# Kernel optimization log

Measured on AMD Instinct MI355X. Metric: run time of the kernel, lower is better.

The kernel has to match this reference:

```python
import jax, jax.numpy as jnp
import numpy as np

V, D_IN = 32000, 300      # vocab, embedding dim (GRU input_size=300)
N, T = 4096, 64           # total nodes across batched graphs, tokens per node
B, NPG = 64, 64           # graphs, nodes per graph
E = 65536                 # total edges (avg degree 16)
RH, GH = 256, 256         # rnn_hidden_dim, gnn_hidden_dim


def gru_cell(x_proj, h, W_hh, b_hh):
    # x_proj = x @ W_ih.T + b_ih, shape [N, 3H]; PyTorch GRU gate order (r, z, n)
    gh = h @ W_hh.T + b_hh
    xr, xz, xn = jnp.split(x_proj, 3, axis=-1)
    hr, hz, hn = jnp.split(gh, 3, axis=-1)
    r = jax.nn.sigmoid(xr + hr)
    z = jax.nn.sigmoid(xz + hz)
    n = jnp.tanh(xn + r * hn)
    return (1.0 - z) * n + z * h


def setup_inputs() -> dict:
    key = jax.random.key(0)
    ks = jax.random.split(key, 16)
    tokens = jax.random.randint(ks[0], (N, T), 0, V)
    # edges live within a single graph (dgl.batch keeps graphs disjoint)
    edge_graph = jnp.arange(E) // (E // B)
    edge_src = edge_graph * NPG + jax.random.randint(ks[1], (E,), 0, NPG)
    edge_dst = edge_graph * NPG + jax.random.randint(ks[2], (E,), 0, NPG)
    graph_id = jnp.arange(N) // NPG
    local = jnp.arange(N) % NPG
    # node types: 0=history, 1=last_sentence (one per graph), 2=response (one per graph)
    node_type = jnp.where(local == NPG - 2, 1, jnp.where(local == NPG - 1, 2, 0))
    s = 0.02
    p = lambda k, shape: jax.random.normal(k, shape, dtype=jnp.float32) * s
    return dict(
        tokens=tokens, edge_src=edge_src, edge_dst=edge_dst,
        graph_id=graph_id, node_type=node_type,
        emb_table=p(ks[3], (V, D_IN)),
        W_ih_f=p(ks[4], (3 * RH, D_IN)), W_hh_f=p(ks[5], (3 * RH, RH)),
        b_ih_f=jnp.zeros((3 * RH,), jnp.float32), b_hh_f=jnp.zeros((3 * RH,), jnp.float32),
        W_ih_b=p(ks[6], (3 * RH, D_IN)), W_hh_b=p(ks[7], (3 * RH, RH)),
        b_ih_b=jnp.zeros((3 * RH,), jnp.float32), b_hh_b=jnp.zeros((3 * RH,), jnp.float32),
        W_g1=p(ks[8], (2 * RH, GH)), b_g1=jnp.zeros((GH,), jnp.float32),
        W_g2=p(ks[9], (GH, GH)), b_g2=jnp.zeros((GH,), jnp.float32),
        W_g3=p(ks[10], (GH, GH)), b_g3=jnp.zeros((GH,), jnp.float32),
        W_g4=p(ks[11], (GH, GH)), b_g4=jnp.zeros((GH,), jnp.float32),
    )


def reference(tokens, edge_src, edge_dst, graph_id, node_type, emb_table,
              W_ih_f, W_hh_f, b_ih_f, b_hh_f,
              W_ih_b, W_hh_b, b_ih_b, b_hh_b,
              W_g1, b_g1, W_g2, b_g2, W_g3, b_g3, W_g4, b_g4):
    x = emb_table[tokens]  # [N, T, 300]
    # Module keeps only output[:, -1, :]:
    #   forward half  = final forward hidden state (full scan over T)
    #   backward half = backward state after processing only timestep T-1
    #                   (i.e. one GRU cell step from zero state) -- exact math.
    xp_f = jnp.einsum('ntd,gd->ntg', x, W_ih_f) + b_ih_f  # [N, T, 3H]
    h0 = jnp.zeros((N, RH), x.dtype)

    def step(h, xp_t):
        return gru_cell(xp_t, h, W_hh_f, b_hh_f), None

    h_fwd, _ = jax.lax.scan(step, h0, jnp.swapaxes(xp_f, 0, 1))
    xp_b = x[:, -1] @ W_ih_b.T + b_ih_b
    h_bwd = gru_cell(xp_b, h0, W_hh_b, b_hh_b)
    h = jnp.concatenate([h_fwd, h_bwd], axis=-1)  # [N, 2H]

    # 4 GCN layers: sum-aggregate neighbor features (copy_src -> sum), then linear + ReLU
    for W, b in ((W_g1, b_g1), (W_g2, b_g2), (W_g3, b_g3), (W_g4, b_g4)):
        agg = jax.ops.segment_sum(h[edge_src], edge_dst, num_segments=N)
        h = jax.nn.relu(agg @ W + b)

    # per-graph readout by node type
    hist_m = (node_type == 0).astype(h.dtype)[:, None]
    last_m = (node_type == 1).astype(h.dtype)[:, None]
    resp_m = (node_type == 2).astype(h.dtype)[:, None]
    hist_sum = jax.ops.segment_sum(h * hist_m, graph_id, num_segments=B)
    hist_cnt = jax.ops.segment_sum(hist_m, graph_id, num_segments=B)
    batched_hist = hist_sum / hist_cnt
    batched_last = jax.ops.segment_sum(h * last_m, graph_id, num_segments=B)
    batched_resp = jax.ops.segment_sum(h * resp_m, graph_id, num_segments=B)
    return (batched_hist, batched_last, batched_resp)
```

## Files before the change

kernel.cpp:

```cpp
#include <hip/hip_runtime.h>
#include <cstddef>

#define NN_ 4096
#define TT_ 64
#define DIN 300
#define DINP 320
#define RH_ 256
#define G3_ 768
#define BB_ 64
#define EE_ 65536

typedef short bf16x8 __attribute__((ext_vector_type(8)));
typedef float f32x4 __attribute__((ext_vector_type(4)));
typedef unsigned short u16;

__device__ __forceinline__ u16 f2bf(float f) {
    unsigned u = __builtin_bit_cast(unsigned, f);
    u += 0x7fff + ((u >> 16) & 1);
    return (u16)(u >> 16);
}
__device__ __forceinline__ float bf2f(u16 v) {
    return __builtin_bit_cast(float, (unsigned)v << 16);
}

__device__ __forceinline__ void gload16(const void* g, void* l) {
    __builtin_amdgcn_global_load_lds(
        (const __attribute__((address_space(1))) unsigned*)g,
        (__attribute__((address_space(3))) unsigned*)l, 16, 0, 0);
}

#define MFMA16 __builtin_amdgcn_mfma_f32_16x16x32_bf16

__global__ void k_zero(float* __restrict__ p, long n) {
    for (long i = (long)blockIdx.x * blockDim.x + threadIdx.x; i < n;
         i += (long)gridDim.x * blockDim.x)
        p[i] = 0.f;
}

__global__ void k_cvt(const float* __restrict__ src, u16* __restrict__ dst,
                      int R, int C, int Cp) {
    long total = (long)R * Cp;
    for (long i = (long)blockIdx.x * blockDim.x + threadIdx.x; i < total;
         i += (long)gridDim.x * blockDim.x) {
        int r = (int)(i / Cp);
        int c = (int)(i - (long)r * Cp);
        dst[i] = (c < C) ? f2bf(src[(size_t)r * C + c]) : (u16)0;
    }
}

__global__ void k_cvtT(const float* __restrict__ W, u16* __restrict__ Wt, int K) {
    int total = 256 * K;
    for (int i = blockIdx.x * blockDim.x + threadIdx.x; i < total;
         i += gridDim.x * blockDim.x) {
        int c = i / K, k = i - c * K;
        Wt[i] = f2bf(W[(size_t)k * 256 + c]);
    }
}

__global__ void k_buildA(const int* __restrict__ src, const int* __restrict__ dst,
                         float* __restrict__ A) {
    int e = blockIdx.x * blockDim.x + threadIdx.x;
    if (e < EE_) {
        int g = src[e] >> 6, i = dst[e] & 63, j = src[e] & 63;
        atomicAdd(&A[(((g << 6) + i) << 6) + j], 1.f);
    }
}

__global__ __launch_bounds__(256) void k_trans(const float* __restrict__ h, int C,
                                               u16* __restrict__ hT) {
    __shared__ u16 Ls[64][72];
    int r0 = blockIdx.x * 64, c0 = blockIdx.y * 64;
    int tid = threadIdx.x;
    int r = tid >> 2, cq = tid & 3;
#pragma unroll
    for (int i = 0; i < 4; i++) {
        float4 v = *(const float4*)(h + (size_t)(r0 + r) * C + c0 + cq * 16 + i * 4);
        Ls[r][cq * 16 + i * 4 + 0] = f2bf(v.x);
        Ls[r][cq * 16 + i * 4 + 1] = f2bf(v.y);
        Ls[r][cq * 16 + i * 4 + 2] = f2bf(v.z);
        Ls[r][cq * 16 + i * 4 + 3] = f2bf(v.w);
    }
    __syncthreads();
    int c = tid >> 2, rq = tid & 3;
    u16 tmp[16];
#pragma unroll
    for (int i = 0; i < 16; i++) tmp[i] = Ls[rq * 16 + i][c];
    u16* o = hT + (size_t)(c0 + c) * NN_ + r0 + rq * 16;
    *(uint4*)o = ((const uint4*)tmp)[0];
    *(uint4*)(o + 8) = ((const uint4*)tmp)[1];
}

__global__ __launch_bounds__(256) void k_xproj(
    const u16* __restrict__ embbf, const u16* __restrict__ Wx,
    const float* __restrict__ bih, const float* __restrict__ bhh,
    u16* __restrict__ XP)
{
    __shared__ __align__(16) u16 As[2][64 * 32];
    __shared__ __align__(16) u16 Bs[2][64 * 32];
    const int tid = threadIdx.x;
    const int v0 = blockIdx.x * 64, c0 = blockIdx.y * 64;
    const int sr = tid >> 2, sq = tid & 3;
    const u16* pa = embbf + (size_t)(v0 + sr) * DINP + sq * 8;
    const u16* pb = Wx + (size_t)(c0 + sr) * DINP + sq * 8;

    const int lane = tid & 63, wave = tid >> 6;
    const int wr = wave >> 1, wc = wave & 1;
    const int l15 = lane & 15, l4 = lane >> 4;
    const int aoff = (wr * 32 + l15) * 32 + l4 * 8;
    const int boff = (wc * 32 + l15) * 32 + l4 * 8;
    f32x4 acc[2][2] = {};

    gload16(pa, &As[0][tid * 8]);
    gload16(pb, &Bs[0][tid * 8]);
    __syncthreads();
    constexpr int NSK = DINP / 32;
#pragma unroll
    for (int s = 0; s < NSK; s++) {
        if (s + 1 < NSK) {
            gload16(pa + (s + 1) * 32, &As[(s + 1) & 1][tid * 8]);
            gload16(pb + (s + 1) * 32, &Bs[(s + 1) & 1][tid * 8]);
        }
        const int b = s & 1;
        bf16x8 a0 = *(const bf16x8*)&As[b][aoff];
        bf16x8 a1 = *(const bf16x8*)&As[b][aoff + 512];
        bf16x8 b0 = *(const bf16x8*)&Bs[b][boff];
        bf16x8 b1 = *(const bf16x8*)&Bs[b][boff + 512];
        acc[0][0] = MFMA16(a0, b0, acc[0][0], 0, 0, 0);
        acc[0][1] = MFMA16(a0, b1, acc[0][1], 0, 0, 0);
        acc[1][0] = MFMA16(a1, b0, acc[1][0], 0, 0, 0);
        acc[1][1] = MFMA16(a1, b1, acc[1][1], 0, 0, 0);
        __syncthreads();
    }
#pragma unroll
    for (int fj = 0; fj < 2; fj++) {
        const int c = c0 + wc * 32 + fj * 16 + l15;
        const float bb = bih[c] + (c < 512 ? bhh[c] : 0.f);
#pragma unroll
        for (int fi = 0; fi < 2; fi++)
#pragma unroll
            for (int rg = 0; rg < 4; rg++) {
                const int v = v0 + wr * 32 + fi * 16 + l4 * 4 + rg;
                XP[(size_t)v * G3_ + c] = f2bf(acc[fi][fj][rg] + bb);
            }
    }
}

__global__ __launch_bounds__(512, 2) void k_scan(
    const int* __restrict__ tokens,
    const u16* __restrict__ XPROJ,
    const u16* __restrict__ Wh,
    const float* __restrict__ bhh,
    float* __restrict__ HA)
{
    __shared__ __align__(16) u16 XPs[16 * G3_];
    __shared__ __align__(16) u16 hS[16 * RH_];
    __shared__ int toks[16 * TT_];

    const int tid = threadIdx.x;
    const int n0 = blockIdx.x * 16;
    const int lane = tid & 63, wave = tid >> 6;
    const int l15 = lane & 15, l4 = lane >> 4;
    const int c0w = wave * 32;

    toks[tid] = tokens[n0 * TT_ + tid];
    toks[512 + tid] = tokens[n0 * TT_ + 512 + tid];
    ((unsigned long long*)hS)[tid] = 0ull;
    ((unsigned long long*)hS)[512 + tid] = 0ull;

    bf16x8 Bv[3][2][8];
#pragma unroll
    for (int g = 0; g < 3; ++g)
#pragma unroll
        for (int f = 0; f < 2; ++f)
#pragma unroll
            for (int ks = 0; ks < 8; ++ks)
                Bv[g][f][ks] = *(const bf16x8*)(
                    Wh + (size_t)(g * 256 + c0w + f * 16 + l15) * RH_ + ks * 32 + l4 * 8);

    const float bhn0 = bhh[512 + c0w + l15];
    const float bhn1 = bhh[512 + c0w + 16 + l15];

    int srow[3], soff[3];
#pragma unroll
    for (int i = 0; i < 3; ++i) {
        int c = tid + i * 512;
        srow[i] = c / 96;
        soff[i] = (c - srow[i] * 96) * 8;
    }
    u16* sdst[3];
#pragma unroll
    for (int i = 0; i < 3; ++i) sdst[i] = XPs + (tid + i * 512) * 8;

    auto STAGE_XP = [&](int t) {
#pragma unroll
        for (int i = 0; i < 3; ++i) {
            int tok = toks[srow[i] * TT_ + t];
            gload16(XPROJ + (size_t)tok * G3_ + soff[i], sdst[i]);
        }
    };

    f32x4 hprev0 = {0.f, 0.f, 0.f, 0.f}, hprev1 = {0.f, 0.f, 0.f, 0.f};

    __syncthreads();

    STAGE_XP(0);
    __syncthreads();

    for (int t = 0; t < TT_; ++t) {
        f32x4 acc[3][2] = {};
#pragma unroll
        for (int ks = 0; ks < 8; ++ks) {
            const int aa = (l15 * 512 + ks * 64 + l4 * 16) ^ ((l15 & 7) << 4);
            bf16x8 a = *(const bf16x8*)((const char*)hS + aa);
#pragma unroll
            for (int g = 0; g < 3; ++g) {
                acc[g][0] = MFMA16(a, Bv[g][0][ks], acc[g][0], 0, 0, 0);
                acc[g][1] = MFMA16(a, Bv[g][1][ks], acc[g][1], 0, 0, 0);
            }
        }
        __syncthreads();

#pragma unroll
        for (int f = 0; f < 2; ++f) {
            const int cc = c0w + f * 16 + l15;
            const float bhn = f == 0 ? bhn0 : bhn1;
#pragma unroll
            for (int rg = 0; rg < 4; ++rg) {
                const int r = l4 * 4 + rg;
                const int xb = r * G3_ + cc;
                float xr = bf2f(XPs[xb]);
                float xz = bf2f(XPs[xb + 256]);
                float xn = bf2f(XPs[xb + 512]);
                float gr = f == 0 ? acc[0][0][rg] : acc[0][1][rg];
                float gz = f == 0 ? acc[1][0][rg] : acc[1][1][rg];
                float gn = f == 0 ? acc[2][0][rg] : acc[2][1][rg];
                float hp = f == 0 ? hprev0[rg] : hprev1[rg];
                float rr = 1.f / (1.f + __expf(-(xr + gr)));
                float zz = 1.f / (1.f + __expf(-(xz + gz)));
                float pre = xn + rr * (gn + bhn);
                float nv = 2.f / (1.f + __expf(-2.f * pre)) - 1.f;
                float hnew = (1.f - zz) * nv + zz * hp;
                if (f == 0) hprev0[rg] = hnew; else hprev1[rg] = hnew;
                if (t < TT_ - 1) {
                    const int ba = (r * 512 + cc * 2) ^ ((r & 7) << 4);
                    *(u16*)((char*)hS + ba) = f2bf(hnew);
                } else {
                    HA[(size_t)(n0 + r) * 512 + cc] = hnew;
                }
            }
        }
        __syncthreads();
        if (t < TT_ - 1) STAGE_XP(t + 1);
    }
}

template<bool XONLY>
__global__ __launch_bounds__(256) void k_step(
    const int* __restrict__ tokens, int t,
    const u16* __restrict__ embbf, const u16* __restrict__ Wx,
    const u16* __restrict__ Wh,
    const float* __restrict__ bih, const float* __restrict__ bhh,
    const u16* __restrict__ hbf_in, const float* __restrict__ hf_in,
    float* __restrict__ outf, int ostride, u16* __restrict__ outbf)
{
    constexpr int NSX = DINP / 32;
    constexpr int NS  = XONLY ? NSX : NSX + RH_ / 32;

    __shared__ __align__(16) u16 As[2][32 * 32];
    __shared__ __align__(16) u16 Bs[2][3 * 64 * 32];

    const int tid = threadIdx.x;
    const int n0 = blockIdx.x * 32;
    const int c0 = blockIdx.y * 64;

    const int sr = tid >> 2;
    const int sq = tid & 3;
    const int tok = (tid < 128) ? tokens[(n0 + sr) * TT_ + t] : 0;
    const u16* ax  = embbf + (size_t)tok * DINP + sq * 8;
    const u16* ah  = XONLY ? ax : hbf_in + (size_t)(n0 + sr) * RH_ + sq * 8;
    const u16* bx0 = Wx + (size_t)(0 * 256 + c0 + sr) * DINP + sq * 8;
    const u16* bx1 = Wx + (size_t)(1 * 256 + c0 + sr) * DINP + sq * 8;
    const u16* bx2 = Wx + (size_t)(2 * 256 + c0 + sr) * DINP + sq * 8;
    const u16* bh0 = XONLY ? ax : Wh + (size_t)(0 * 256 + c0 + sr) * RH_ + sq * 8;
    const u16* bh1 = XONLY ? ax : Wh + (size_t)(1 * 256 + c0 + sr) * RH_ + sq * 8;
    const u16* bh2 = XONLY ? ax : Wh + (size_t)(2 * 256 + c0 + sr) * RH_ + sq * 8;

    auto STAGE = [&](int b, int s) {
        u16* db = &Bs[b][tid * 8];
        if (s < NSX) {
            int kk = s * 32;
            if (tid < 128) gload16(ax + kk, &As[b][tid * 8]);
            gload16(bx0 + kk, db);
            gload16(bx1 + kk, db + 2048);
            gload16(bx2 + kk, db + 4096);
        } else {
            int kk = (s - NSX) * 32;
            if (tid < 128) gload16(ah + kk, &As[b][tid * 8]);
            gload16(bh0 + kk, db);
            gload16(bh1 + kk, db + 2048);
            gload16(bh2 + kk, db + 4096);
        }
    };

    const int lane = tid & 63;
    const int wave = tid >> 6;
    const int wr = wave >> 1, wc = wave & 1;
    const int l15 = lane & 15, l4 = lane >> 4;

    f32x4 aR[2] = {}, aZ[2] = {}, aXN[2] = {}, aHN[2] = {};

    const int aoff = (wr * 16 + l15) * 32 + l4 * 8;
    const int boff = (wc * 32 + l15) * 32 + l4 * 8;

    auto COMPUTE = [&](int b, bool xp) {
        bf16x8 a0 = *(const bf16x8*)&As[b][aoff];
        const u16* B = &Bs[b][0];
        bf16x8 r0 = *(const bf16x8*)&B[boff];
        bf16x8 r1 = *(const bf16x8*)&B[boff + 512];
        bf16x8 z0 = *(const bf16x8*)&B[2048 + boff];
        bf16x8 z1 = *(const bf16x8*)&B[2048 + boff + 512];
        bf16x8 n0f = *(const bf16x8*)&B[4096 + boff];
        bf16x8 n1f = *(const bf16x8*)&B[4096 + boff + 512];
        aR[0] = MFMA16(a0, r0, aR[0], 0, 0, 0);
        aR[1] = MFMA16(a0, r1, aR[1], 0, 0, 0);
        aZ[0] = MFMA16(a0, z0, aZ[0], 0, 0, 0);
        aZ[1] = MFMA16(a0, z1, aZ[1], 0, 0, 0);
        if (xp) {
            aXN[0] = MFMA16(a0, n0f, aXN[0], 0, 0, 0);
            aXN[1] = MFMA16(a0, n1f, aXN[1], 0, 0, 0);
        } else {
            aHN[0] = MFMA16(a0, n0f, aHN[0], 0, 0, 0);
            aHN[1] = MFMA16(a0, n1f, aHN[1], 0, 0, 0);
        }
    };

    STAGE(0, 0);
    __syncthreads();
#pragma unroll
    for (int s = 0; s < NS; ++s) {
        if (s + 1 < NS) STAGE((s + 1) & 1, s + 1);
        COMPUTE(s & 1, s < NSX);
        __syncthreads();
    }

#pragma unroll
    for (int fj = 0; fj < 2; ++fj) {
        const int c = c0 + wc * 32 + fj * 16 + l15;
        const float bR  = bih[c] + bhh[c];
        const float bZ  = bih[256 + c] + bhh[256 + c];
        const float bXN = bih[512 + c];
        const float bHN = bhh[512 + c];
#pragma unroll
        for (int rg = 0; rg < 4; ++rg) {
            const int n = n0 + wr * 16 + l4 * 4 + rg;
            float r  = 1.f / (1.f + __expf(-(aR[fj][rg] + bR)));
            float z  = 1.f / (1.f + __expf(-(aZ[fj][rg] + bZ)));
            float pre = aXN[fj][rg] + bXN + r * (aHN[fj][rg] + bHN);
            float nv = 2.f / (1.f + __expf(-2.f * pre)) - 1.f;
            float hp = XONLY ? 0.f : hf_in[(size_t)n * RH_ + c];
            float h  = (1.f - z) * nv + z * hp;
            outf[(size_t)n * ostride + c] = h;
            if (!XONLY) outbf[(size_t)n * RH_ + c] = f2bf(h);
        }
    }
}

__global__ __launch_bounds__(256) void k_agg(
    const u16* __restrict__ Abf, const u16* __restrict__ hT,
    u16* __restrict__ aggbf, int C)
{
    const int g = blockIdx.x, ct = blockIdx.y;
    const int lane = threadIdx.x & 63, wave = threadIdx.x >> 6;
    const int wi = wave >> 1, wcC = wave & 1;
    const int l15 = lane & 15, l4 = lane >> 4;
    f32x4 acc[2][2] = {};
#pragma unroll
    for (int kc = 0; kc < 2; kc++) {
        bf16x8 af[2], bf_[2];
#pragma unroll
        for (int fi = 0; fi < 2; fi++)
            af[fi] = *(const bf16x8*)(Abf + ((size_t)g * 64 + wi * 32 + fi * 16 + l15) * 64
                                      + kc * 32 + l4 * 8);
#pragma unroll
        for (int fj = 0; fj < 2; fj++)
            bf_[fj] = *(const bf16x8*)(hT + (size_t)(ct * 64 + wcC * 32 + fj * 16 + l15) * NN_
                                       + g * 64 + kc * 32 + l4 * 8);
#pragma unroll
        for (int fi = 0; fi < 2; fi++)
#pragma unroll
            for (int fj = 0; fj < 2; fj++)
                acc[fi][fj] = MFMA16(af[fi], bf_[fj], acc[fi][fj], 0, 0, 0);
    }
#pragma unroll
    for (int fi = 0; fi < 2; fi++)
#pragma unroll
        for (int fj = 0; fj < 2; fj++)
#pragma unroll
            for (int rg = 0; rg < 4; rg++) {
                int n = g * 64 + wi * 32 + fi * 16 + l4 * 4 + rg;
                int c = ct * 64 + wcC * 32 + fj * 16 + l15;
                aggbf[(size_t)n * C + c] = f2bf(acc[fi][fj][rg]);
            }
}

template<int K>
__global__ __launch_bounds__(256) void k_gcnM(
    const u16* __restrict__ Ag, const u16* __restrict__ Wt,
    const float* __restrict__ bias, float* __restrict__ outF)
{
    __shared__ __align__(16) u16 As[2][64 * 32];
    __shared__ __align__(16) u16 Bs[2][64 * 32];
    const int tid = threadIdx.x;
    const int n0 = blockIdx.x * 64, c0 = blockIdx.y * 64;
    const int sr = tid >> 2, sq = tid & 3;
    const u16* pa = Ag + (size_t)(n0 + sr) * K + sq * 8;
    const u16* pb = Wt + (size_t)(c0 + sr) * K + sq * 8;

    const int lane = tid & 63, wave = tid >> 6;
    const int wr = wave >> 1, wc = wave & 1;
    const int l15 = lane & 15, l4 = lane >> 4;
    const int aoff = (wr * 32 + l15) * 32 + l4 * 8;
    const int boff = (wc * 32 + l15) * 32 + l4 * 8;
    f32x4 acc[2][2] = {};

    gload16(pa, &As[0][tid * 8]);
    gload16(pb, &Bs[0][tid * 8]);
    __syncthreads();
    constexpr int NSK = K / 32;
#pragma unroll
    for (int s = 0; s < NSK; s++) {
        if (s + 1 < NSK) {
            gload16(pa + (s + 1) * 32, &As[(s + 1) & 1][tid * 8]);
            gload16(pb + (s + 1) * 32, &Bs[(s + 1) & 1][tid * 8]);
        }
        const int b = s & 1;
        bf16x8 a0 = *(const bf16x8*)&As[b][aoff];
        bf16x8 a1 = *(const bf16x8*)&As[b][aoff + 512];
        bf16x8 b0 = *(const bf16x8*)&Bs[b][boff];
        bf16x8 b1 = *(const bf16x8*)&Bs[b][boff + 512];
        acc[0][0] = MFMA16(a0, b0, acc[0][0], 0, 0, 0);
        acc[0][1] = MFMA16(a0, b1, acc[0][1], 0, 0, 0);
        acc[1][0] = MFMA16(a1, b0, acc[1][0], 0, 0, 0);
        acc[1][1] = MFMA16(a1, b1, acc[1][1], 0, 0, 0);
        __syncthreads();
    }
#pragma unroll
    for (int fj = 0; fj < 2; fj++) {
        const int c = c0 + wc * 32 + fj * 16 + l15;
        const float bb = bias[c];
#pragma unroll
        for (int fi = 0; fi < 2; fi++)
#pragma unroll
            for (int rg = 0; rg < 4; rg++) {
                const int n = n0 + wr * 32 + fi * 16 + l4 * 4 + rg;
                outF[(size_t)n * 256 + c] = fmaxf(acc[fi][fj][rg] + bb, 0.f);
            }
    }
}

__global__ void k_readout(const float* __restrict__ h, const int* __restrict__ gid,
                          const int* __restrict__ ntype, float* __restrict__ out,
                          float* __restrict__ cnt)
{
    for (int idx = blockIdx.x * blockDim.x + threadIdx.x; idx < NN_ * 256;
         idx += gridDim.x * blockDim.x) {
        int n = idx >> 8, c = idx & 255;
        float v = h[idx];
        int g = gid[n], t = ntype[n];
        if (t == 0) {
            atomicAdd(&out[g * 256 + c], v);
            if (c == 0) atomicAdd(&cnt[g], 1.f);
        } else if (t == 1) {
            atomicAdd(&out[16384 + g * 256 + c], v);
        } else {
            atomicAdd(&out[32768 + g * 256 + c], v);
        }
    }
}

__global__ void k_finalize(float* __restrict__ out, const float* __restrict__ cnt)
{
    int idx = blockIdx.x * blockDim.x + threadIdx.x;
    out[idx] /= cnt[idx >> 8];
}

extern "C" void kernel_launch(void* const* d_in, const int* in_sizes, int n_in,
                              void* d_out, int out_size, void* d_ws, size_t ws_size,
                              hipStream_t stream)
{
    const int*   tokens = (const int*)d_in[0];
    const int*   esrc   = (const int*)d_in[1];
    const int*   edst   = (const int*)d_in[2];
    const int*   gid    = (const int*)d_in[3];
    const int*   ntype  = (const int*)d_in[4];
    const float* emb    = (const float*)d_in[5];
    const float* W_ih_f = (const float*)d_in[6];
    const float* W_hh_f = (const float*)d_in[7];
    const float* b_ih_f = (const float*)d_in[8];
    const float* b_hh_f = (const float*)d_in[9];
    const float* W_ih_b = (const float*)d_in[10];
    const float* b_ih_b = (const float*)d_in[12];
    const float* b_hh_b = (const float*)d_in[13];
    const float* Wg[4]  = {(const float*)d_in[14], (const float*)d_in[16],
                           (const float*)d_in[18], (const float*)d_in[20]};
    const float* bg[4]  = {(const float*)d_in[15], (const float*)d_in[17],
                           (const float*)d_in[19], (const float*)d_in[21]};
    float* out = (float*)d_out;

    float* hF    = (float*)d_ws;
    u16*   embbf = (u16*)(hF + (size_t)NN_ * RH_);
    u16*   wxf   = embbf + 32000L * DINP;
    u16*   whf   = wxf + (size_t)G3_ * DINP;
    u16*   wxb   = whf + (size_t)G3_ * RH_;
    u16*   wtg   = wxb + (size_t)G3_ * DINP;
    u16*   Abf   = wtg + 256L * 512;
    u16*   hT    = Abf + 64L * 64 * 64;
    u16*   aggb  = hT + 512L * NN_;
    u16*   XPROJ = aggb + (size_t)NN_ * 512;
    float* Af    = (float*)(XPROJ + 32000L * G3_);
    float* HA    = Af + 64L * 64 * 64;
    float* CNT   = HA + (size_t)NN_ * 512;

    k_cvt<<<2048, 256, 0, stream>>>(emb, embbf, 32000, DIN, DINP);
    k_cvt<<<256, 256, 0, stream>>>(W_ih_f, wxf, G3_, DIN, DINP);
    k_cvt<<<256, 256, 0, stream>>>(W_hh_f, whf, G3_, RH_, RH_);
    k_cvt<<<256, 256, 0, stream>>>(W_ih_b, wxb, G3_, DIN, DINP);
    k_zero<<<256, 256, 0, stream>>>(Af, 64L * 64 * 64);
    k_buildA<<<256, 256, 0, stream>>>(esrc, edst, Af);
    k_cvt<<<256, 256, 0, stream>>>(Af, Abf, 64 * 64, 64, 64);

    k_xproj<<<dim3(500, 12), 256, 0, stream>>>(embbf, wxf, b_ih_f, b_hh_f, XPROJ);
    k_scan<<<256, 512, 0, stream>>>(tokens, XPROJ, whf, b_hh_f, HA);

    k_step<true><<<dim3(128, 4), 256, 0, stream>>>(
        tokens, TT_ - 1, embbf, wxb, nullptr, b_ih_b, b_hh_b,
        nullptr, nullptr, HA + 256, 512, nullptr);

    k_trans<<<dim3(64, 8), 256, 0, stream>>>(HA, 512, hT);
    for (int l = 0; l < 4; l++) {
        int K = (l == 0) ? 512 : 256;
        k_cvtT<<<128, 256, 0, stream>>>(Wg[l], wtg, K);
        k_agg<<<dim3(64, K / 64), 256, 0, stream>>>(Abf, hT, aggb, K);
        if (K == 512)
            k_gcnM<512><<<dim3(64, 4), 256, 0, stream>>>(aggb, wtg, bg[l], hF);
        else
            k_gcnM<256><<<dim3(64, 4), 256, 0, stream>>>(aggb, wtg, bg[l], hF);
        if (l < 3) k_trans<<<dim3(64, 4), 256, 0, stream>>>(hF, 256, hT);
    }

    k_zero<<<256, 256, 0, stream>>>(out, 49152);
    k_zero<<<1, 64, 0, stream>>>(CNT, 64);
    k_readout<<<2048, 256, 0, stream>>>(hF, gid, ntype, out, CNT);
    k_finalize<<<64, 256, 0, stream>>>(out, CNT);
}
```

Before: 400.0 us.

## Interleave XPROJ gates per column and load directly into registers in GRU scan

Reorders the precomputed input projection so the r/z/n values of each hidden column sit together (padded to 4 halves). The scan kernel then fetches them straight into registers with one 8-byte load per element and prefetches the next step before the barrier, which removes the LDS staging buffer and the global-to-LDS copy. The LDS swizzle for the hidden state is also changed and workspace buffers are aliased. The price is a larger XPROJ buffer (4 slots per column instead of 3) and uncoalesced scattered register loads on the serial critical path.

```diff
diff --git a/kernel.cpp b/kernel.cpp
--- a/kernel.cpp
+++ b/kernel.cpp
@@ -13,6 +13,7 @@
 typedef short bf16x8 __attribute__((ext_vector_type(8)));
 typedef float f32x4 __attribute__((ext_vector_type(4)));
 typedef unsigned short u16;
+typedef unsigned short u16x4 __attribute__((ext_vector_type(4)));
 
 __device__ __forceinline__ u16 f2bf(float f) {
     unsigned u = __builtin_bit_cast(unsigned, f);
@@ -93,7 +94,7 @@
 __global__ __launch_bounds__(256) void k_xproj(
     const u16* __restrict__ embbf, const u16* __restrict__ Wx,
     const float* __restrict__ bih, const float* __restrict__ bhh,
-    u16* __restrict__ XP)
+    u16* __restrict__ XP2)
 {
     __shared__ __align__(16) u16 As[2][64 * 32];
     __shared__ __align__(16) u16 Bs[2][64 * 32];
@@ -133,28 +134,29 @@
     }
 #pragma unroll
     for (int fj = 0; fj < 2; fj++) {
-        const int c = c0 + wc * 32 + fj * 16 + l15;
-        const float bb = bih[c] + (c < 512 ? bhh[c] : 0.f);
+        const int cf = c0 + wc * 32 + fj * 16 + l15;
+        const int g = cf >> 8, c = cf & 255;
+        const float bb = bih[cf] + (cf < 512 ? bhh[cf] : 0.f);
 #pragma unroll
         for (int fi = 0; fi < 2; fi++)
 #pragma unroll
             for (int rg = 0; rg < 4; rg++) {
                 const int v = v0 + wr * 32 + fi * 16 + l4 * 4 + rg;
-                XP[(size_t)v * G3_ + c] = f2bf(acc[fi][fj][rg] + bb);
+                XP2[((size_t)v * 256 + c) * 4 + g] = f2bf(acc[fi][fj][rg] + bb);
             }
     }
 }
 
-__global__ __launch_bounds__(512, 2) void k_scan(
+__global__ __launch_bounds__(512) __attribute__((amdgpu_waves_per_eu(2, 2)))
+void k_scan(
     const int* __restrict__ tokens,
-    const u16* __restrict__ XPROJ,
+    const u16* __restrict__ XP2,
     const u16* __restrict__ Wh,
     const float* __restrict__ bhh,
     float* __restrict__ HA)
 {
-    __shared__ __align__(16) u16 XPs[16 * G3_];
     __shared__ __align__(16) u16 hS[16 * RH_];
-    __shared__ int toks[16 * TT_];
+    __shared__ int toks[16 * 68];
 
     const int tid = threadIdx.x;
     const int n0 = blockIdx.x * 16;
@@ -162,8 +164,10 @@
     const int l15 = lane & 15, l4 = lane >> 4;
     const int c0w = wave * 32;
 
-    toks[tid] = tokens[n0 * TT_ + tid];
-    toks[512 + tid] = tokens[n0 * TT_ + 512 + tid];
+    for (int idx = tid; idx < 16 * TT_; idx += 512) {
+        int row = idx >> 6, tt = idx & 63;
+        toks[row * 68 + tt] = tokens[(n0 + row) * TT_ + tt];
+    }
     ((unsigned long long*)hS)[tid] = 0ull;
     ((unsigned long long*)hS)[512 + tid] = 0ull;
 
@@ -180,37 +184,25 @@
     const float bhn0 = bhh[512 + c0w + l15];
     const float bhn1 = bhh[512 + c0w + 16 + l15];
 
-    int srow[3], soff[3];
-#pragma unroll
-    for (int i = 0; i < 3; ++i) {
-        int c = tid + i * 512;
-        srow[i] = c / 96;
-        soff[i] = (c - srow[i] * 96) * 8;
-    }
-    u16* sdst[3];
-#pragma unroll
-    for (int i = 0; i < 3; ++i) sdst[i] = XPs + (tid + i * 512) * 8;
-
-    auto STAGE_XP = [&](int t) {
-#pragma unroll
-        for (int i = 0; i < 3; ++i) {
-            int tok = toks[srow[i] * TT_ + t];
-            gload16(XPROJ + (size_t)tok * G3_ + soff[i], sdst[i]);
-        }
-    };
-
-    f32x4 hprev0 = {0.f, 0.f, 0.f, 0.f}, hprev1 = {0.f, 0.f, 0.f, 0.f};
-
     __syncthreads();
 
-    STAGE_XP(0);
-    __syncthreads();
-
+    u16x4 xp[2][4];
+#pragma unroll
+    for (int f = 0; f < 2; ++f)
+#pragma unroll
+        for (int rg = 0; rg < 4; ++rg) {
+            int tok = toks[(l4 * 4 + rg) * 68];
+            xp[f][rg] = *(const u16x4*)(XP2 + ((size_t)tok * 256 + c0w + f * 16 + l15) * 4);
+        }
+
+    f32x4 hprev[2] = {};
+
+#pragma unroll 1
     for (int t = 0; t < TT_; ++t) {
         f32x4 acc[3][2] = {};
 #pragma unroll
         for (int ks = 0; ks < 8; ++ks) {
-            const int aa = (l15 * 512 + ks * 64 + l4 * 16) ^ ((l15 & 7) << 4);
+            const int aa = (l15 * 512 + ks * 64 + l4 * 16) ^ (((l15 >> 2) & 3) << 5);
             bf16x8 a = *(const bf16x8*)((const char*)hS + aa);
 #pragma unroll
             for (int g = 0; g < 3; ++g) {
@@ -227,30 +219,36 @@
 #pragma unroll
             for (int rg = 0; rg < 4; ++rg) {
                 const int r = l4 * 4 + rg;
-                const int xb = r * G3_ + cc;
-                float xr = bf2f(XPs[xb]);
-                float xz = bf2f(XPs[xb + 256]);
-                float xn = bf2f(XPs[xb + 512]);
-                float gr = f == 0 ? acc[0][0][rg] : acc[0][1][rg];
-                float gz = f == 0 ? acc[1][0][rg] : acc[1][1][rg];
-                float gn = f == 0 ? acc[2][0][rg] : acc[2][1][rg];
-                float hp = f == 0 ? hprev0[rg] : hprev1[rg];
+                float xr = bf2f(xp[f][rg][0]);
+                float xz = bf2f(xp[f][rg][1]);
+                float xn = bf2f(xp[f][rg][2]);
+                float gr = acc[0][f][rg];
+                float gz = acc[1][f][rg];
+                float gn = acc[2][f][rg];
+                float hp = hprev[f][rg];
                 float rr = 1.f / (1.f + __expf(-(xr + gr)));
                 float zz = 1.f / (1.f + __expf(-(xz + gz)));
                 float pre = xn + rr * (gn + bhn);
                 float nv = 2.f / (1.f + __expf(-2.f * pre)) - 1.f;
                 float hnew = (1.f - zz) * nv + zz * hp;
-                if (f == 0) hprev0[rg] = hnew; else hprev1[rg] = hnew;
+                hprev[f][rg] = hnew;
                 if (t < TT_ - 1) {
-                    const int ba = (r * 512 + cc * 2) ^ ((r & 7) << 4);
+                    const int ba = (r * 512 + cc * 2) ^ (((r >> 2) & 3) << 5);
                     *(u16*)((char*)hS + ba) = f2bf(hnew);
                 } else {
                     HA[(size_t)(n0 + r) * 512 + cc] = hnew;
                 }
             }
         }
+        const int tn = (t + 1 < TT_) ? t + 1 : TT_ - 1;
+#pragma unroll
+        for (int f = 0; f < 2; ++f)
+#pragma unroll
+            for (int rg = 0; rg < 4; ++rg) {
+                int tok = toks[(l4 * 4 + rg) * 68 + tn];
+                xp[f][rg] = *(const u16x4*)(XP2 + ((size_t)tok * 256 + c0w + f * 16 + l15) * 4);
+            }
         __syncthreads();
-        if (t < TT_ - 1) STAGE_XP(t + 1);
     }
 }
 
@@ -508,17 +506,17 @@
     float* out = (float*)d_out;
 
     float* hF    = (float*)d_ws;
+    float* Af    = hF;
     u16*   embbf = (u16*)(hF + (size_t)NN_ * RH_);
     u16*   wxf   = embbf + 32000L * DINP;
     u16*   whf   = wxf + (size_t)G3_ * DINP;
     u16*   wxb   = whf + (size_t)G3_ * RH_;
     u16*   wtg   = wxb + (size_t)G3_ * DINP;
     u16*   Abf   = wtg + 256L * 512;
-    u16*   hT    = Abf + 64L * 64 * 64;
+    u16*   XP2   = Abf + 64L * 64 * 64;
+    u16*   hT    = XP2;
     u16*   aggb  = hT + 512L * NN_;
-    u16*   XPROJ = aggb + (size_t)NN_ * 512;
-    float* Af    = (float*)(XPROJ + 32000L * G3_);
-    float* HA    = Af + 64L * 64 * 64;
+    float* HA    = (float*)(XP2 + 32000L * 1024);
     float* CNT   = HA + (size_t)NN_ * 512;
 
     k_cvt<<<2048, 256, 0, stream>>>(emb, embbf, 32000, DIN, DINP);
@@ -529,8 +527,8 @@
     k_buildA<<<256, 256, 0, stream>>>(esrc, edst, Af);
     k_cvt<<<256, 256, 0, stream>>>(Af, Abf, 64 * 64, 64, 64);
 
-    k_xproj<<<dim3(500, 12), 256, 0, stream>>>(embbf, wxf, b_ih_f, b_hh_f, XPROJ);
-    k_scan<<<256, 512, 0, stream>>>(tokens, XPROJ, whf, b_hh_f, HA);
+    k_xproj<<<dim3(500, 12), 256, 0, stream>>>(embbf, wxf, b_ih_f, b_hh_f, XP2);
+    k_scan<<<256, 512, 0, stream>>>(tokens, XP2, whf, b_hh_f, HA);
 
     k_step<true><<<dim3(128, 4), 256, 0, stream>>>(
         tokens, TT_ - 1, embbf, wxb, nullptr, b_ih_b, b_hh_b,
```

New measurement: 587.4 us. +46.9%, slower.

## Restructure GRU scan XP staging layout, pin weights in AGPRs, alias workspace

Applied to the files above, without the earlier changes.

The scan kernel now stages the per-step input projection into three gate-separated, XOR-swizzled LDS planes with one token lookup per thread, and pads the token table to avoid bank conflicts. The recurrent weight fragments are forced into accumulation registers through an asm constraint, and the time loop is no longer unrolled. The workspace is compacted so Af aliases hF and hT aliases XPROJ, shrinking the memory footprint. The goal is fewer LDS bank conflicts, fewer address computations, and lower register pressure in the latency-bound recurrent loop, at the cost of relying on buffer aliasing being safe with respect to lifetimes.

```diff
diff --git a/kernel.cpp b/kernel.cpp
--- a/kernel.cpp
+++ b/kernel.cpp
@@ -152,9 +152,9 @@
     const float* __restrict__ bhh,
     float* __restrict__ HA)
 {
-    __shared__ __align__(16) u16 XPs[16 * G3_];
     __shared__ __align__(16) u16 hS[16 * RH_];
-    __shared__ int toks[16 * TT_];
+    __shared__ __align__(16) u16 XPs[3 * 16 * 256];
+    __shared__ int toks[16 * 68];
 
     const int tid = threadIdx.x;
     const int n0 = blockIdx.x * 16;
@@ -162,8 +162,10 @@
     const int l15 = lane & 15, l4 = lane >> 4;
     const int c0w = wave * 32;
 
-    toks[tid] = tokens[n0 * TT_ + tid];
-    toks[512 + tid] = tokens[n0 * TT_ + 512 + tid];
+    for (int idx = tid; idx < 16 * TT_; idx += 512) {
+        int row = idx >> 6, tt = idx & 63;
+        toks[row * 68 + tt] = tokens[(n0 + row) * TT_ + tt];
+    }
     ((unsigned long long*)hS)[tid] = 0ull;
     ((unsigned long long*)hS)[512 + tid] = 0ull;
 
@@ -173,41 +175,37 @@
 #pragma unroll
         for (int f = 0; f < 2; ++f)
 #pragma unroll
-            for (int ks = 0; ks < 8; ++ks)
+            for (int ks = 0; ks < 8; ++ks) {
                 Bv[g][f][ks] = *(const bf16x8*)(
                     Wh + (size_t)(g * 256 + c0w + f * 16 + l15) * RH_ + ks * 32 + l4 * 8);
+                asm("" : "+a"(Bv[g][f][ks]));
+            }
 
     const float bhn0 = bhh[512 + c0w + l15];
     const float bhn1 = bhh[512 + c0w + 16 + l15];
 
-    int srow[3], soff[3];
-#pragma unroll
-    for (int i = 0; i < 3; ++i) {
-        int c = tid + i * 512;
-        srow[i] = c / 96;
-        soff[i] = (c - srow[i] * 96) * 8;
-    }
-    u16* sdst[3];
-#pragma unroll
-    for (int i = 0; i < 3; ++i) sdst[i] = XPs + (tid + i * 512) * 8;
+    const int srow = tid >> 5, sch = tid & 31;
+    const int ssw = (((sch * 16) ^ ((srow >> 2) << 5)) >> 1);
 
     auto STAGE_XP = [&](int t) {
-#pragma unroll
-        for (int i = 0; i < 3; ++i) {
-            int tok = toks[srow[i] * TT_ + t];
-            gload16(XPROJ + (size_t)tok * G3_ + soff[i], sdst[i]);
-        }
+        int tok = toks[srow * 68 + t];
+        const u16* src = XPROJ + (size_t)tok * G3_ + ssw;
+#pragma unroll
+        for (int g = 0; g < 3; ++g)
+            gload16(src + g * 256, XPs + g * 4096 + tid * 8);
     };
 
-    f32x4 hprev0 = {0.f, 0.f, 0.f, 0.f}, hprev1 = {0.f, 0.f, 0.f, 0.f};
-
     __syncthreads();
 
     STAGE_XP(0);
-    __syncthreads();
-
+
+    f32x4 hprev[2] = {};
+
+#pragma unroll 1
     for (int t = 0; t < TT_; ++t) {
-        f32x4 acc[3][2] = {};
+        f32x4 acc[3][2];
+#pragma unroll
+        for (int g = 0; g < 3; ++g) { acc[g][0] = f32x4{}; acc[g][1] = f32x4{}; }
 #pragma unroll
         for (int ks = 0; ks < 8; ++ks) {
             const int aa = (l15 * 512 + ks * 64 + l4 * 16) ^ ((l15 & 7) << 4);
@@ -227,20 +225,20 @@
 #pragma unroll
             for (int rg = 0; rg < 4; ++rg) {
                 const int r = l4 * 4 + rg;
-                const int xb = r * G3_ + cc;
+                const int xb = r * 256 + ((((cc * 2) ^ ((r >> 2) << 5))) >> 1);
                 float xr = bf2f(XPs[xb]);
-                float xz = bf2f(XPs[xb + 256]);
-                float xn = bf2f(XPs[xb + 512]);
-                float gr = f == 0 ? acc[0][0][rg] : acc[0][1][rg];
-                float gz = f == 0 ? acc[1][0][rg] : acc[1][1][rg];
-                float gn = f == 0 ? acc[2][0][rg] : acc[2][1][rg];
-                float hp = f == 0 ? hprev0[rg] : hprev1[rg];
+                float xz = bf2f(XPs[4096 + xb]);
+                float xn = bf2f(XPs[8192 + xb]);
+                float gr = acc[0][f][rg];
+                float gz = acc[1][f][rg];
+                float gn = acc[2][f][rg];
+                float hp = hprev[f][rg];
                 float rr = 1.f / (1.f + __expf(-(xr + gr)));
                 float zz = 1.f / (1.f + __expf(-(xz + gz)));
                 float pre = xn + rr * (gn + bhn);
                 float nv = 2.f / (1.f + __expf(-2.f * pre)) - 1.f;
                 float hnew = (1.f - zz) * nv + zz * hp;
-                if (f == 0) hprev0[rg] = hnew; else hprev1[rg] = hnew;
+                hprev[f][rg] = hnew;
                 if (t < TT_ - 1) {
                     const int ba = (r * 512 + cc * 2) ^ ((r & 7) << 4);
                     *(u16*)((char*)hS + ba) = f2bf(hnew);
@@ -508,17 +506,17 @@
     float* out = (float*)d_out;
 
     float* hF    = (float*)d_ws;
+    float* Af    = hF;
     u16*   embbf = (u16*)(hF + (size_t)NN_ * RH_);
     u16*   wxf   = embbf + 32000L * DINP;
     u16*   whf   = wxf + (size_t)G3_ * DINP;
     u16*   wxb   = whf + (size_t)G3_ * RH_;
     u16*   wtg   = wxb + (size_t)G3_ * DINP;
     u16*   Abf   = wtg + 256L * 512;
-    u16*   hT    = Abf + 64L * 64 * 64;
+    u16*   XPROJ = Abf + 64L * 64 * 64;
+    u16*   hT    = XPROJ;
     u16*   aggb  = hT + 512L * NN_;
-    u16*   XPROJ = aggb + (size_t)NN_ * 512;
-    float* Af    = (float*)(XPROJ + 32000L * G3_);
-    float* HA    = Af + 64L * 64 * 64;
+    float* HA    = (float*)(XPROJ + 32000L * G3_);
     float* CNT   = HA + (size_t)NN_ * 512;
 
     k_cvt<<<2048, 256, 0, stream>>>(emb, embbf, 32000, DIN, DINP);
```

Measured after the change: 528.1 us. +32.0%, slower.
